# Kernel optimization log

Hardware: AMD Instinct MI355X
Metric: run time of the kernel (lower is better)

Reference implementation:

```python
import jax, jax.numpy as jnp
import numpy as np

NUM_WORDS = 1024
EMBED_DIM = 1024
NUM_SAMPLES = 65536


def setup_inputs() -> dict:
    key = jax.random.key(0)
    k1, k2, k3, k4 = jax.random.split(key, 4)
    return {
        "word_embeddings": jax.random.normal(k1, (NUM_WORDS, EMBED_DIM), dtype=jnp.float32),
        "t_query": jax.random.uniform(k2, (NUM_SAMPLES,), dtype=jnp.float32),
        "tension_params": jax.random.normal(k3, (NUM_WORDS - 1,), dtype=jnp.float32),
        "semantic_weights": jnp.ones((EMBED_DIM,), dtype=jnp.float32),
        "word_biases": jax.random.normal(k4, (NUM_WORDS, EMBED_DIM), dtype=jnp.float32),
        "curvature_controls": jnp.ones((NUM_WORDS,), dtype=jnp.float32),
    }


def reference(word_embeddings, t_query, tension_params, semantic_weights, word_biases, curvature_controls):
    N, D = word_embeddings.shape
    # adjusted + semantic weighting
    emb = (word_embeddings + word_biases) * semantic_weights[None, :]  # [N, D]

    # t_words = linspace(0, 1, N): segment index = floor(t * (N-1)), clipped to [0, N-2]
    scaled = t_query * (N - 1)
    seg = jnp.clip(jnp.floor(scaled).astype(jnp.int32), 0, N - 2)  # [S]
    t = scaled - seg.astype(t_query.dtype)  # local parameter in [0, 1]

    # control points via batched gather
    p0 = emb[jnp.maximum(seg - 1, 0)]       # [S, D]
    p1 = emb[seg]
    p2 = emb[seg + 1]
    p3 = emb[jnp.minimum(seg + 2, N - 1)]

    tension = jax.nn.sigmoid(tension_params[seg])  # [S]
    c1 = curvature_controls[seg]
    c2 = curvature_controls[seg + 1]

    t2 = t * t
    t3 = t2 * t
    v0 = (-0.5 * t3 + t2 - 0.5 * t) * tension
    v1 = (1.5 * t3 - 2.5 * t2 + 1.0) * c1
    v2 = (-1.5 * t3 + 2.0 * t2 + 0.5 * t) * c2
    v3 = (0.5 * t3 - 0.5 * t2) * tension
    total = v0 + v1 + v2 + v3
    v0, v1, v2, v3 = v0 / total, v1 / total, v2 / total, v3 / total

    out = (v0[:, None] * p0 + v1[:, None] * p1 + v2[:, None] * p2 + v3[:, None] * p3)  # [S, D]

    # boundary handling: t <= 0 -> emb[0], t >= 1 -> emb[-1]
    out = jnp.where((t_query <= 0.0)[:, None], emb[0][None, :], out)
    out = jnp.where((t_query >= 1.0)[:, None], emb[-1][None, :], out)
    return out
```

## Files before the change

### kernel.cpp

```cpp
#include <hip/hip_runtime.h>
#include <hip/hip_bf16.h>
#include <math.h>

#define NUM_WORDS 1024
#define EMBED_DIM 1024
#define NUM_SAMPLES 65536

__global__ __launch_bounds__(256) void emb_precompute_kernel(
    const float4* __restrict__ we,
    const float4* __restrict__ wb,
    const float4* __restrict__ sw,
    float4* __restrict__ emb)
{
    int i = blockIdx.x * blockDim.x + threadIdx.x;
    int col4 = i & 255;
    float4 w = we[i];
    float4 b = wb[i];
    float4 s = sw[col4];
    float4 r;
    r.x = (w.x + b.x) * s.x;
    r.y = (w.y + b.y) * s.y;
    r.z = (w.z + b.z) * s.z;
    r.w = (w.w + b.w) * s.w;
    emb[i] = r;
}

__global__ __launch_bounds__(256) void spline_kernel(
    const float* __restrict__ emb,
    const float* __restrict__ t_query,
    const float* __restrict__ tension_p,
    const float* __restrict__ curv,
    float* __restrict__ out)
{
    const int s = blockIdx.x;
    const float tq = t_query[s];

    float scaled = tq * (float)(NUM_WORDS - 1);
    int seg = (int)floorf(scaled);
    seg = min(max(seg, 0), NUM_WORDS - 2);
    float t = scaled - (float)seg;

    int r0 = max(seg - 1, 0);
    int r1 = seg;
    int r2 = seg + 1;
    int r3 = min(seg + 2, NUM_WORDS - 1);

    float tension = 1.0f / (1.0f + __expf(-tension_p[seg]));
    float c1 = curv[seg];
    float c2 = curv[seg + 1];
    float t2 = t * t;
    float t3 = t2 * t;
    float v0 = (-0.5f * t3 + t2 - 0.5f * t) * tension;
    float v1 = (1.5f * t3 - 2.5f * t2 + 1.0f) * c1;
    float v2 = (-1.5f * t3 + 2.0f * t2 + 0.5f * t) * c2;
    float v3 = (0.5f * t3 - 0.5f * t2) * tension;
    float total = v0 + v1 + v2 + v3;
    float inv = 1.0f / total;
    v0 *= inv; v1 *= inv; v2 *= inv; v3 *= inv;

    if (tq <= 0.0f) { v0 = 1.0f; v1 = 0.0f; v2 = 0.0f; v3 = 0.0f; r0 = 0; }
    else if (tq >= 1.0f) { v0 = 1.0f; v1 = 0.0f; v2 = 0.0f; v3 = 0.0f; r0 = NUM_WORDS - 1; }

    const int tid = threadIdx.x;
    const float4* p0 = (const float4*)(emb + (size_t)r0 * EMBED_DIM);
    const float4* p1 = (const float4*)(emb + (size_t)r1 * EMBED_DIM);
    const float4* p2 = (const float4*)(emb + (size_t)r2 * EMBED_DIM);
    const float4* p3 = (const float4*)(emb + (size_t)r3 * EMBED_DIM);

    float4 a = p0[tid];
    float4 b = p1[tid];
    float4 c = p2[tid];
    float4 d = p3[tid];

    float4 r;
    r.x = v0 * a.x + v1 * b.x + v2 * c.x + v3 * d.x;
    r.y = v0 * a.y + v1 * b.y + v2 * c.y + v3 * d.y;
    r.z = v0 * a.z + v1 * b.z + v2 * c.z + v3 * d.z;
    r.w = v0 * a.w + v1 * b.w + v2 * c.w + v3 * d.w;

    float4* orow = (float4*)(out + (size_t)s * EMBED_DIM);
    orow[tid] = r;
}

extern "C" void kernel_launch(void* const* d_in, const int* in_sizes, int n_in,
                              void* d_out, int out_size, void* d_ws, size_t ws_size,
                              hipStream_t stream) {
    const float* we = (const float*)d_in[0];
    const float* tq = (const float*)d_in[1];
    const float* tp = (const float*)d_in[2];
    const float* sw = (const float*)d_in[3];
    const float* wb = (const float*)d_in[4];
    const float* cc = (const float*)d_in[5];
    float* out = (float*)d_out;

    float* emb = (float*)d_ws;

    emb_precompute_kernel<<<1024, 256, 0, stream>>>(
        (const float4*)we, (const float4*)wb, (const float4*)sw, (float4*)emb);

    spline_kernel<<<NUM_SAMPLES, 256, 0, stream>>>(emb, tq, tp, cc, out);
}
```

Baseline: 321.9 us.

## Bucket samples by segment so each block reuses four control rows from registers

Replaces the one-block-per-sample gather with a counting sort of samples by segment: a histogram kernel, a scan, and a scatter that computes the per-sample weights. An output kernel assigned to each segment then loads its four embedding rows once into registers and streams out every sample in that bucket. This removes the repeated 16 KB gather per sample, which was heavy on L2 traffic. In exchange it adds three small launches, atomics, and load imbalance when buckets are uneven. The t>=1 boundary is now expressed through the weight on row seg+1.

```diff
diff --git a/kernel.cpp b/kernel.cpp
--- a/kernel.cpp
+++ b/kernel.cpp
@@ -2,21 +2,30 @@
 #include <hip/hip_bf16.h>
 #include <math.h>
 
-#define NUM_WORDS 1024
-#define EMBED_DIM 1024
-#define NUM_SAMPLES 65536
+#define NW 1024
+#define ED 1024
+#define NS 65536
+#define ED4 (ED / 4)
+#define CHUNKS 4
+#define BATCH 128
+
+#define EMB_OFF  0
+#define WTS_OFF  (4u * 1024u * 1024u)
+#define IDS_OFF  (WTS_OFF + NS * 16u)
+#define CNT_OFF  (IDS_OFF + NS * 4u)
+#define OFF_OFF  (CNT_OFF + NW * 4u)
+#define CUR_OFF  (OFF_OFF + (NW + 1) * 4u)
 
 __global__ __launch_bounds__(256) void emb_precompute_kernel(
-    const float4* __restrict__ we,
-    const float4* __restrict__ wb,
-    const float4* __restrict__ sw,
-    float4* __restrict__ emb)
+    const float4* __restrict__ we, const float4* __restrict__ wb,
+    const float4* __restrict__ sw, float4* __restrict__ emb,
+    int* __restrict__ counts)
 {
-    int i = blockIdx.x * blockDim.x + threadIdx.x;
-    int col4 = i & 255;
+    int i = blockIdx.x * 256 + threadIdx.x;
+    if (i < NW) counts[i] = 0;
     float4 w = we[i];
     float4 b = wb[i];
-    float4 s = sw[col4];
+    float4 s = sw[i & (ED4 - 1)];
     float4 r;
     r.x = (w.x + b.x) * s.x;
     r.y = (w.y + b.y) * s.y;
@@ -25,61 +34,111 @@
     emb[i] = r;
 }
 
-__global__ __launch_bounds__(256) void spline_kernel(
-    const float* __restrict__ emb,
-    const float* __restrict__ t_query,
-    const float* __restrict__ tension_p,
-    const float* __restrict__ curv,
-    float* __restrict__ out)
+__device__ __forceinline__ int seg_of(float q) {
+    float scaled = q * (float)(NW - 1);
+    int seg = (int)floorf(scaled);
+    return min(max(seg, 0), NW - 2);
+}
+
+__global__ __launch_bounds__(256) void hist_kernel(
+    const float* __restrict__ tq, int* __restrict__ counts)
 {
-    const int s = blockIdx.x;
-    const float tq = t_query[s];
+    int s = blockIdx.x * 256 + threadIdx.x;
+    atomicAdd(&counts[seg_of(tq[s])], 1);
+}
 
-    float scaled = tq * (float)(NUM_WORDS - 1);
+__global__ __launch_bounds__(1024) void scan_kernel(
+    const int* __restrict__ counts, int* __restrict__ offs,
+    int* __restrict__ curs)
+{
+    __shared__ int tmp[NW];
+    int tid = threadIdx.x;
+    int v = counts[tid];
+    tmp[tid] = v;
+    __syncthreads();
+    for (int d = 1; d < NW; d <<= 1) {
+        int add = (tid >= d) ? tmp[tid - d] : 0;
+        __syncthreads();
+        tmp[tid] += add;
+        __syncthreads();
+    }
+    int incl = tmp[tid];
+    offs[tid + 1] = incl;
+    curs[tid] = incl - v;
+    if (tid == 0) offs[0] = 0;
+}
+
+__global__ __launch_bounds__(256) void scatter_kernel(
+    const float* __restrict__ tq, const float* __restrict__ tp,
+    const float* __restrict__ cc, int* __restrict__ curs,
+    int* __restrict__ ids, float4* __restrict__ wts)
+{
+    int s = blockIdx.x * 256 + threadIdx.x;
+    float q = tq[s];
+    float scaled = q * (float)(NW - 1);
     int seg = (int)floorf(scaled);
-    seg = min(max(seg, 0), NUM_WORDS - 2);
+    seg = min(max(seg, 0), NW - 2);
     float t = scaled - (float)seg;
 
-    int r0 = max(seg - 1, 0);
-    int r1 = seg;
-    int r2 = seg + 1;
-    int r3 = min(seg + 2, NUM_WORDS - 1);
-
-    float tension = 1.0f / (1.0f + __expf(-tension_p[seg]));
-    float c1 = curv[seg];
-    float c2 = curv[seg + 1];
-    float t2 = t * t;
-    float t3 = t2 * t;
+    float tension = 1.0f / (1.0f + expf(-tp[seg]));
+    float c1 = cc[seg], c2 = cc[seg + 1];
+    float t2 = t * t, t3 = t2 * t;
     float v0 = (-0.5f * t3 + t2 - 0.5f * t) * tension;
     float v1 = (1.5f * t3 - 2.5f * t2 + 1.0f) * c1;
     float v2 = (-1.5f * t3 + 2.0f * t2 + 0.5f * t) * c2;
     float v3 = (0.5f * t3 - 0.5f * t2) * tension;
-    float total = v0 + v1 + v2 + v3;
-    float inv = 1.0f / total;
+    float inv = 1.0f / (v0 + v1 + v2 + v3);
     v0 *= inv; v1 *= inv; v2 *= inv; v3 *= inv;
 
-    if (tq <= 0.0f) { v0 = 1.0f; v1 = 0.0f; v2 = 0.0f; v3 = 0.0f; r0 = 0; }
-    else if (tq >= 1.0f) { v0 = 1.0f; v1 = 0.0f; v2 = 0.0f; v3 = 0.0f; r0 = NUM_WORDS - 1; }
+    if (q <= 0.0f) { v0 = 1.0f; v1 = 0.0f; v2 = 0.0f; v3 = 0.0f; }
+    if (q >= 1.0f) { v0 = 0.0f; v1 = 0.0f; v2 = 1.0f; v3 = 0.0f; }
 
+    int pos = atomicAdd(&curs[seg], 1);
+    ids[pos] = s;
+    wts[pos] = make_float4(v0, v1, v2, v3);
+}
+
+__global__ __launch_bounds__(256) void out_kernel(
+    const float4* __restrict__ emb4, const int* __restrict__ offs,
+    const int* __restrict__ ids, const float4* __restrict__ wts,
+    float4* __restrict__ out4)
+{
+    __shared__ int    s_ids[BATCH];
+    __shared__ float4 s_w[BATCH];
+
+    const int seg   = blockIdx.x >> 2;
+    const int chunk = blockIdx.x & (CHUNKS - 1);
+    const int beg = offs[seg];
+    const int end = offs[seg + 1];
     const int tid = threadIdx.x;
-    const float4* p0 = (const float4*)(emb + (size_t)r0 * EMBED_DIM);
-    const float4* p1 = (const float4*)(emb + (size_t)r1 * EMBED_DIM);
-    const float4* p2 = (const float4*)(emb + (size_t)r2 * EMBED_DIM);
-    const float4* p3 = (const float4*)(emb + (size_t)r3 * EMBED_DIM);
 
-    float4 a = p0[tid];
-    float4 b = p1[tid];
-    float4 c = p2[tid];
-    float4 d = p3[tid];
+    const int r0 = max(seg - 1, 0);
+    const int r3 = min(seg + 2, NW - 1);
+    float4 a = emb4[r0 * ED4 + tid];
+    float4 b = emb4[seg * ED4 + tid];
+    float4 c = emb4[(seg + 1) * ED4 + tid];
+    float4 d = emb4[r3 * ED4 + tid];
 
-    float4 r;
-    r.x = v0 * a.x + v1 * b.x + v2 * c.x + v3 * d.x;
-    r.y = v0 * a.y + v1 * b.y + v2 * c.y + v3 * d.y;
-    r.z = v0 * a.z + v1 * b.z + v2 * c.z + v3 * d.z;
-    r.w = v0 * a.w + v1 * b.w + v2 * c.w + v3 * d.w;
-
-    float4* orow = (float4*)(out + (size_t)s * EMBED_DIM);
-    orow[tid] = r;
+    for (int base = beg + chunk; base < end; base += CHUNKS * BATCH) {
+        int nb = min(BATCH, (end - base + CHUNKS - 1) / CHUNKS);
+        __syncthreads();
+        if (tid < nb) {
+            int idx = base + CHUNKS * tid;
+            s_ids[tid] = ids[idx];
+            s_w[tid]   = wts[idx];
+        }
+        __syncthreads();
+        for (int k = 0; k < nb; ++k) {
+            float4 w  = s_w[k];
+            int   sid = s_ids[k];
+            float4 r;
+            r.x = w.x * a.x + w.y * b.x + w.z * c.x + w.w * d.x;
+            r.y = w.x * a.y + w.y * b.y + w.z * c.y + w.w * d.y;
+            r.z = w.x * a.z + w.y * b.z + w.z * c.z + w.w * d.z;
+            r.w = w.x * a.w + w.y * b.w + w.z * c.w + w.w * d.w;
+            out4[(size_t)sid * ED4 + tid] = r;
+        }
+    }
 }
 
 extern "C" void kernel_launch(void* const* d_in, const int* in_sizes, int n_in,
@@ -93,10 +152,24 @@
     const float* cc = (const float*)d_in[5];
     float* out = (float*)d_out;
 
-    float* emb = (float*)d_ws;
+    char* ws = (char*)d_ws;
+    float*  emb    = (float*)(ws + EMB_OFF);
+    float4* wts    = (float4*)(ws + WTS_OFF);
+    int*    ids    = (int*)(ws + IDS_OFF);
+    int*    counts = (int*)(ws + CNT_OFF);
+    int*    offs   = (int*)(ws + OFF_OFF);
+    int*    curs   = (int*)(ws + CUR_OFF);
 
     emb_precompute_kernel<<<1024, 256, 0, stream>>>(
-        (const float4*)we, (const float4*)wb, (const float4*)sw, (float4*)emb);
+        (const float4*)we, (const float4*)wb, (const float4*)sw,
+        (float4*)emb, counts);
 
-    spline_kernel<<<NUM_SAMPLES, 256, 0, stream>>>(emb, tq, tp, cc, out);
+    hist_kernel<<<NS / 256, 256, 0, stream>>>(tq, counts);
+
+    scan_kernel<<<1, 1024, 0, stream>>>(counts, offs, curs);
+
+    scatter_kernel<<<NS / 256, 256, 0, stream>>>(tq, tp, cc, curs, ids, wts);
+
+    out_kernel<<<NW * CHUNKS, 256, 0, stream>>>(
+        (const float4*)emb, offs, ids, wts, (float4*)out);
 }
```

Result: faster. 315.0 us (-2.2%).
